# Optimization experiments

Hardware: AMD Instinct MI355X
Metric: run time of the kernel (lower is better)

## Reference

```python
import jax, jax.numpy as jnp
import numpy as np

NUM_CLASSES = 21
NEGPOS_RATIO = 3
B, P = 64, 24564


def setup_inputs() -> dict:
    key = jax.random.key(0)
    ks = jax.random.split(key, 10)
    return {
        "loc_data": jax.random.normal(ks[0], (B, P, 4), jnp.float32),
        "conf_data": jax.random.normal(ks[1], (B, P, NUM_CLASSES), jnp.float32),
        "has_lp_data": jax.random.normal(ks[2], (B, P, 2), jnp.float32),
        "size_lp_data": jax.random.normal(ks[3], (B, P, 2), jnp.float32),
        "offset_data": jax.random.normal(ks[4], (B, P, 2), jnp.float32),
        "loc_t": jax.random.normal(ks[5], (B, P, 4), jnp.float32),
        "conf_t": jax.random.randint(ks[6], (B, P), 0, NUM_CLASSES, jnp.int64),
        "has_lp_t": jax.random.randint(ks[7], (B, P), 0, 2, jnp.int64),
        "size_lp_t": jax.random.normal(ks[8], (B, P, 2), jnp.float32),
        "offset_t": jax.random.normal(ks[9], (B, P, 2), jnp.float32),
    }


def _smooth_l1_sum(p, t, mask):
    # sum-reduced smooth L1 (beta=1) over elements selected by mask
    d = jnp.abs(p - t)
    l = jnp.where(d < 1.0, 0.5 * d * d, d - 0.5)
    return jnp.sum(l * mask)


def _ce_per_row(logits, labels):
    # per-row cross entropy: logsumexp(logits) - logits[label]
    lse = jax.nn.logsumexp(logits, axis=-1)
    g = jnp.take_along_axis(logits, labels[..., None], axis=-1)[..., 0]
    return lse - g


def reference(loc_data, conf_data, has_lp_data, size_lp_data, offset_data,
              loc_t, conf_t, has_lp_t, size_lp_t, offset_t):
    dt = loc_data.dtype
    num_priors = conf_data.shape[1]
    pos = conf_t > 0                                  # [B,P]
    posf = pos.astype(dt)[..., None]                  # [B,P,1]

    # localization loss over positives
    loss_l = _smooth_l1_sum(loc_data, loc_t, posf)

    # size / offset losses over positives, gated by has_lp flag
    hlp = has_lp_t.astype(dt)[..., None]              # [B,P,1]
    loss_size_lp = _smooth_l1_sum(size_lp_data * hlp, size_lp_t * hlp, posf)
    loss_offset = _smooth_l1_sum(offset_data * hlp, offset_t * hlp, posf)

    # hard negative mining on per-prior conf CE
    ce = _ce_per_row(conf_data, conf_t)               # [B,P]
    ce_mine = jnp.where(pos, 0.0, ce)
    loss_idx = jnp.argsort(-ce_mine, axis=1)          # descending sort indices
    idx_rank = jnp.argsort(loss_idx, axis=1)          # rank of each prior
    num_pos = jnp.sum(pos, axis=1, keepdims=True)     # [B,1]
    num_neg = jnp.clip(NEGPOS_RATIO * num_pos, None, num_priors - 1)
    neg = idx_rank < num_neg                          # [B,P]
    sel = (pos | neg).astype(dt)

    loss_c = jnp.sum(ce * sel)
    loss_has_lp = jnp.sum(_ce_per_row(has_lp_data, has_lp_t) * sel)

    N = jnp.sum(pos).astype(dt)
    return (loss_l / N, loss_c / N, loss_size_lp / N,
            loss_offset / N, loss_has_lp / N)
```

## Files before the change

### kernel.cpp

```cpp
#include <hip/hip_runtime.h>
#include <stdint.h>

#define NC 21
#define BATCH 64
#define PRI 24564
#define NROWS (BATCH * PRI)
#define SLABS 32
#define SLABR 768
#define GBLK (BATCH * SLABS)
#define SENT 0xFFFFFFFFu

typedef float f4a4 __attribute__((ext_vector_type(4), aligned(4)));

__device__ __forceinline__ float sl1f(float p, float t) {
    float d = fabsf(p - t);
    return d < 1.0f ? 0.5f * d * d : d - 0.5f;
}

__device__ __forceinline__ unsigned int f2k(float v) {
    unsigned int u = __float_as_uint(v);
    return (u & 0x80000000u) ? ~u : (u | 0x80000000u);
}

__device__ __forceinline__ unsigned int chkey(float2 ch) {
    unsigned hb = __float_as_uint(ch.y);
    return (hb & 0x80000000u) ? 0x80000000u : f2k(ch.x);
}

__device__ __forceinline__ double blockReduce(double v, double* sred) {
    #pragma unroll
    for (int off = 32; off > 0; off >>= 1)
        v += __shfl_down(v, off, 64);
    const int wid = threadIdx.x >> 6, lane = threadIdx.x & 63;
    __syncthreads();
    if (lane == 0) sred[wid] = v;
    __syncthreads();
    double r = 0.0;
    if (threadIdx.x == 0) r = sred[0] + sred[1] + sred[2] + sred[3];
    return r;
}

__global__ __launch_bounds__(256, 4) void k_main(
    const float* __restrict__ loc_data, const float* __restrict__ conf_data,
    const float* __restrict__ has_lp_data, const float* __restrict__ size_lp_data,
    const float* __restrict__ offset_data, const float* __restrict__ loc_t,
    const int* __restrict__ conf_t, const int* __restrict__ has_lp_t,
    const float* __restrict__ size_lp_t, const float* __restrict__ offset_t,
    float2* __restrict__ ws_ch, int* __restrict__ numpos, double* __restrict__ part,
    int* __restrict__ ghist1)
{
    __shared__ int hist[4096];
    __shared__ double sred[4];
    const int tid = threadIdx.x;
    const int b = blockIdx.x >> 5, s = blockIdx.x & 31;
    for (int k = tid; k < 4096; k += 256) hist[k] = 0;
    __syncthreads();

    int pr[3]; bool vld[3];
    #pragma unroll
    for (int i = 0; i < 3; ++i) {
        int p = s * SLABR + i * 256 + tid;
        vld[i] = p < PRI;
        pr[i] = vld[i] ? p : PRI - 1;
    }
    const unsigned rb = (unsigned)b * PRI;

    int ct[3];
    #pragma unroll
    for (int i = 0; i < 3; ++i) ct[i] = conf_t[rb + pr[i]];
    f4a4 cw[3][5]; float c20[3], gg[3];
    #pragma unroll
    for (int i = 0; i < 3; ++i) {
        const float* crow = conf_data + (long)(rb + pr[i]) * NC;
        #pragma unroll
        for (int j = 0; j < 5; ++j) cw[i][j] = ((const f4a4*)crow)[j];
        c20[i] = crow[20];
        gg[i] = crow[ct[i]];
    }
    float ce[3];
    #pragma unroll
    for (int i = 0; i < 3; ++i) {
        float m = c20[i];
        #pragma unroll
        for (int j = 0; j < 5; ++j)
            m = fmaxf(m, fmaxf(fmaxf(cw[i][j].x, cw[i][j].y), fmaxf(cw[i][j].z, cw[i][j].w)));
        float sum = __expf(c20[i] - m);
        #pragma unroll
        for (int j = 0; j < 5; ++j)
            sum += __expf(cw[i][j].x - m) + __expf(cw[i][j].y - m)
                 + __expf(cw[i][j].z - m) + __expf(cw[i][j].w - m);
        ce[i] = m + __logf(sum) - gg[i];
    }
    #pragma unroll
    for (int i = 0; i < 3; ++i) {
        if (vld[i] && ct[i] <= 0) {
            unsigned key = f2k(ce[i]);
            if (key != 0x80000000u) atomicAdd(&hist[key >> 20], 1);
        }
    }

    int hl[3]; float4 lp[3], lt[3]; float2 sp2[3], st2[3], op2[3], ot2[3], hh[3];
    #pragma unroll
    for (int i = 0; i < 3; ++i) {
        const unsigned r = rb + pr[i];
        hl[i] = has_lp_t[r];
        lp[i] = ((const float4*)loc_data)[r];
        lt[i] = ((const float4*)loc_t)[r];
        sp2[i] = ((const float2*)size_lp_data)[r];
        st2[i] = ((const float2*)size_lp_t)[r];
        op2[i] = ((const float2*)offset_data)[r];
        ot2[i] = ((const float2*)offset_t)[r];
        hh[i] = ((const float2*)has_lp_data)[r];
    }
    double aL = 0.0, aS = 0.0, aO = 0.0;
    int myp = 0;
    #pragma unroll
    for (int i = 0; i < 3; ++i) {
        const bool pos = ct[i] > 0;
        float ll = sl1f(lp[i].x, lt[i].x) + sl1f(lp[i].y, lt[i].y)
                 + sl1f(lp[i].z, lt[i].z) + sl1f(lp[i].w, lt[i].w);
        float ls = sl1f(sp2[i].x, st2[i].x) + sl1f(sp2[i].y, st2[i].y);
        float lo = sl1f(op2[i].x, ot2[i].x) + sl1f(op2[i].y, ot2[i].y);
        const float pf = (vld[i] && pos) ? 1.f : 0.f;
        const float hf = (hl[i] != 0) ? 1.f : 0.f;
        aL += (double)(pf * ll);
        aS += (double)(pf * hf * ls);
        aO += (double)(pf * hf * lo);
        float hm = fmaxf(hh[i].x, hh[i].y);
        float hs = __expf(hh[i].x - hm) + __expf(hh[i].y - hm);
        float hlce = fmaxf(hm + __logf(hs) - (hl[i] != 0 ? hh[i].y : hh[i].x), 0.0f);
        unsigned hb = __float_as_uint(hlce) | (pos ? 0x80000000u : 0u);
        if (vld[i]) ws_ch[rb + pr[i]] = make_float2(ce[i], __uint_as_float(hb));
        myp += (vld[i] && pos) ? 1 : 0;
    }

    double v;
    v = blockReduce(aL, sred); if (tid == 0) part[0 * GBLK + blockIdx.x] = v;
    v = blockReduce(aS, sred); if (tid == 0) part[1 * GBLK + blockIdx.x] = v;
    v = blockReduce(aO, sred); if (tid == 0) part[2 * GBLK + blockIdx.x] = v;
    v = blockReduce((double)myp, sred);
    if (tid == 0 && v > 0.0) atomicAdd(&numpos[b], (int)(v + 0.5));

    __syncthreads();
    for (int k = tid; k < 4096; k += 256) {
        int h = hist[k];
        if (h) atomicAdd(&ghist1[(b << 12) + k], h);
    }
}

__global__ __launch_bounds__(256) void k_pick0(
    const int* __restrict__ ghist1, const int* __restrict__ numpos,
    unsigned* __restrict__ prefix_io, int* __restrict__ rem_io,
    unsigned* __restrict__ selT, int* __restrict__ needed)
{
    const int b = blockIdx.x, tid = threadIdx.x;
    __shared__ int sct[256];
    __shared__ unsigned s_dig;
    __shared__ int s_rem;

    int K = 3 * numpos[b]; if (K > PRI - 1) K = PRI - 1;

    int h[16];
    const int* g = ghist1 + (b << 12) + tid * 16;
    int ctn = 0;
    #pragma unroll
    for (int j = 0; j < 16; ++j) { h[j] = g[j]; ctn += h[j]; }
    sct[tid] = ctn;
    __syncthreads();
    #pragma unroll
    for (int off = 1; off < 256; off <<= 1) {
        int v = (tid + off < 256) ? sct[tid + off] : 0;
        __syncthreads();
        sct[tid] += v;
        __syncthreads();
    }
    const int M = sct[0];

    if (K <= 0) {
        if (tid == 0) { selT[b] = 0xFFFFFFFFu; needed[b] = 0; rem_io[b] = 0; prefix_io[b] = SENT; }
        return;
    }
    if (K > M) {
        if (tid == 0) { selT[b] = 0x80000000u; needed[b] = K - M; rem_io[b] = 0; prefix_io[b] = SENT; }
        return;
    }
    const int Safter = (tid < 255) ? sct[tid + 1] : 0;
    int cum = Safter;
    #pragma unroll
    for (int j = 15; j >= 0; --j) {
        int c2 = cum + h[j];
        if (c2 >= K && cum < K) { s_dig = (unsigned)(tid * 16 + j); s_rem = K - cum; }
        cum = c2;
    }
    __syncthreads();
    if (tid == 0) { prefix_io[b] = s_dig; rem_io[b] = s_rem; }
}

template<int MSHIFT, int BSHIFT>
__global__ __launch_bounds__(256) void k_hist(
    const float2* __restrict__ ws_ch, const unsigned* __restrict__ prefix_io,
    int* __restrict__ ghist)
{
    const int b = blockIdx.x >> 5, s = blockIdx.x & 31;
    const unsigned pref = prefix_io[b];
    if (pref == SENT) return;
    __shared__ int hist[1024];
    const int tid = threadIdx.x;
    for (int k = tid; k < 1024; k += 256) hist[k] = 0;
    __syncthreads();
    #pragma unroll
    for (int i = 0; i < 3; ++i) {
        const int p = s * SLABR + i * 256 + tid;
        if (p < PRI) {
            unsigned key = chkey(ws_ch[(unsigned)b * PRI + p]);
            if (key != 0x80000000u && (key >> MSHIFT) == pref)
                atomicAdd(&hist[(key >> BSHIFT) & 1023], 1);
        }
    }
    __syncthreads();
    for (int k = tid; k < 1024; k += 256) {
        int h = hist[k];
        if (h) atomicAdd(&ghist[(b << 10) + k], h);
    }
}

template<int ROUND>
__global__ __launch_bounds__(256) void k_pickR(
    const int* __restrict__ ghist, unsigned* __restrict__ prefix_io,
    int* __restrict__ rem_io, unsigned* __restrict__ selT, int* __restrict__ needed)
{
    const int b = blockIdx.x, tid = threadIdx.x;
    const int rem = rem_io[b];
    if (rem <= 0) return;
    __shared__ int sct[256];
    __shared__ unsigned s_dig;
    __shared__ int s_rem;
    int h[4];
    const int* g = ghist + (b << 10) + tid * 4;
    int ctn = 0;
    #pragma unroll
    for (int j = 0; j < 4; ++j) { h[j] = g[j]; ctn += h[j]; }
    sct[tid] = ctn;
    __syncthreads();
    #pragma unroll
    for (int off = 1; off < 256; off <<= 1) {
        int v = (tid + off < 256) ? sct[tid + off] : 0;
        __syncthreads();
        sct[tid] += v;
        __syncthreads();
    }
    const int Safter = (tid < 255) ? sct[tid + 1] : 0;
    int cum = Safter;
    #pragma unroll
    for (int j = 3; j >= 0; --j) {
        int c2 = cum + h[j];
        if (c2 >= rem && cum < rem) { s_dig = (unsigned)(tid * 4 + j); s_rem = rem - cum; }
        cum = c2;
    }
    __syncthreads();
    if (tid == 0) {
        if (ROUND == 1) { prefix_io[b] = (prefix_io[b] << 10) | s_dig; rem_io[b] = s_rem; }
        else            { selT[b] = (prefix_io[b] << 10) | s_dig;      needed[b] = s_rem; }
    }
}

__global__ __launch_bounds__(256) void k_sel2(
    const float2* __restrict__ ws_ch, const unsigned* __restrict__ selT,
    int* __restrict__ cntT, double* __restrict__ sums)
{
    __shared__ double sred[4];
    const int tid = threadIdx.x;
    const int b = blockIdx.x >> 5, s = blockIdx.x & 31;
    const unsigned T = selT[b];
    double aC = 0.0, aH = 0.0, tC = 0.0, tH = 0.0, cc = 0.0;
    #pragma unroll
    for (int i = 0; i < 3; ++i) {
        const int p = s * SLABR + i * 256 + tid;
        if (p < PRI) {
            float2 ch = ws_ch[(unsigned)b * PRI + p];
            unsigned hb = __float_as_uint(ch.y);
            const bool pos = (hb >> 31) != 0;
            const unsigned key = pos ? 0x80000000u : f2k(ch.x);
            const float hlv = __uint_as_float(hb & 0x7fffffffu);
            if (pos || key > T) { aC += (double)ch.x; aH += (double)hlv; }
            if (key == T) {
                cc += 1.0;
                if (!pos) { tC += (double)ch.x; tH += (double)hlv; }
            }
        }
    }
    double v;
    v = blockReduce(aC, sred); if (tid == 0) sums[0 * GBLK + blockIdx.x] = v;
    v = blockReduce(aH, sred); if (tid == 0) sums[1 * GBLK + blockIdx.x] = v;
    v = blockReduce(tC, sred); if (tid == 0) sums[2 * GBLK + blockIdx.x] = v;
    v = blockReduce(tH, sred); if (tid == 0) sums[3 * GBLK + blockIdx.x] = v;
    v = blockReduce(cc, sred); if (tid == 0) cntT[blockIdx.x] = (int)(v + 0.5);
}

__global__ __launch_bounds__(256) void k_cut(
    const float2* __restrict__ ws_ch, const unsigned* __restrict__ selT,
    const int* __restrict__ needed, const int* __restrict__ cntT,
    const double* __restrict__ sums, double* __restrict__ lossCH)
{
    const int b = blockIdx.x, tid = threadIdx.x;
    __shared__ double sred[4];
    __shared__ int scnt_s[32];
    __shared__ int s_sl, s_loc, s_found;
    __shared__ int wtot[4];
    const int need = needed[b];
    const unsigned T = selT[b];

    if (tid < 32) scnt_s[tid] = cntT[b * 32 + tid];
    __syncthreads();
    if (tid == 0) {
        int sl = 32, loc = 0, cum = 0;
        if (need > 0) {
            for (int s2 = 0; s2 < 32; ++s2) {
                int c2 = scnt_s[s2];
                if (cum + c2 >= need) { sl = s2; loc = need - cum; break; }
                cum += c2;
            }
        }
        s_sl = sl; s_loc = loc; s_found = -1;
    }
    __syncthreads();
    const int sl = s_sl, loc = s_loc;

    double aC = 0.0, aH = 0.0;
    if (tid < 32) {
        aC = sums[0 * GBLK + b * 32 + tid] + (tid < sl ? sums[2 * GBLK + b * 32 + tid] : 0.0);
        aH = sums[1 * GBLK + b * 32 + tid] + (tid < sl ? sums[3 * GBLK + b * 32 + tid] : 0.0);
    }
    double totC = blockReduce(aC, sred);
    double totH = blockReduce(aH, sred);

    if (sl < 32) {
        int run = 0;
        for (int i = 0; i < 3; ++i) {
            const int p = sl * SLABR + i * 256 + tid;
            bool eq = false;
            if (p < PRI) eq = (chkey(ws_ch[(unsigned)b * PRI + p]) == T);
            const unsigned long long m = __ballot(eq);
            const int lane = tid & 63, wid = tid >> 6;
            if (lane == 0) wtot[wid] = __popcll(m);
            const int mex = __popcll(m & ((1ull << lane) - 1ull));
            __syncthreads();
            int woff = 0;
            for (int w = 0; w < wid; ++w) woff += wtot[w];
            if (eq && (run + woff + mex + 1 == loc)) s_found = p;
            __syncthreads();
            run += wtot[0] + wtot[1] + wtot[2] + wtot[3];
            __syncthreads();
        }
        const int cutoff = s_found;
        double pC = 0.0, pH = 0.0;
        for (int i = 0; i < 3; ++i) {
            const int p = sl * SLABR + i * 256 + tid;
            if (p < PRI && p <= cutoff) {
                float2 ch = ws_ch[(unsigned)b * PRI + p];
                unsigned hb = __float_as_uint(ch.y);
                const bool pos = (hb >> 31) != 0;
                const unsigned key = pos ? 0x80000000u : f2k(ch.x);
                if (!pos && key == T) {
                    pC += (double)ch.x;
                    pH += (double)__uint_as_float(hb & 0x7fffffffu);
                }
            }
        }
        double v1 = blockReduce(pC, sred);
        double v2 = blockReduce(pH, sred);
        if (tid == 0) { totC += v1; totH += v2; }
    }
    if (tid == 0) { lossCH[b] = totC; lossCH[64 + b] = totH; }
}

__global__ __launch_bounds__(256) void k_final(
    const double* __restrict__ part, const int* __restrict__ numpos,
    const double* __restrict__ lossCH, float* __restrict__ out)
{
    __shared__ double sred[4];
    const int tid = threadIdx.x;
    double s[3];
    #pragma unroll
    for (int k = 0; k < 3; ++k) {
        double a = 0.0;
        for (int t = tid; t < GBLK; t += 256) a += part[k * GBLK + t];
        s[k] = blockReduce(a, sred);
    }
    double lc = (tid < BATCH) ? lossCH[tid] : 0.0;
    lc = blockReduce(lc, sred);
    double lh = (tid < BATCH) ? lossCH[64 + tid] : 0.0;
    lh = blockReduce(lh, sred);
    double n = (tid < BATCH) ? (double)numpos[tid] : 0.0;
    n = blockReduce(n, sred);
    if (tid == 0) {
        out[0] = (float)(s[0] / n);
        out[1] = (float)(lc / n);
        out[2] = (float)(s[1] / n);
        out[3] = (float)(s[2] / n);
        out[4] = (float)(lh / n);
    }
}

extern "C" void kernel_launch(void* const* d_in, const int* in_sizes, int n_in,
                              void* d_out, int out_size, void* d_ws, size_t ws_size,
                              hipStream_t stream)
{
    const float* loc_data     = (const float*)d_in[0];
    const float* conf_data    = (const float*)d_in[1];
    const float* has_lp_data  = (const float*)d_in[2];
    const float* size_lp_data = (const float*)d_in[3];
    const float* offset_data  = (const float*)d_in[4];
    const float* loc_t        = (const float*)d_in[5];
    const int*   conf_t       = (const int*)d_in[6];
    const int*   has_lp_t     = (const int*)d_in[7];
    const float* size_lp_t    = (const float*)d_in[8];
    const float* offset_t     = (const float*)d_in[9];
    float* out = (float*)d_out;

    char* ws = (char*)d_ws;
    int* numpos      = (int*)(ws + 0);
    unsigned* selT   = (unsigned*)(ws + 256);
    int* needed      = (int*)(ws + 512);
    unsigned* prefix = (unsigned*)(ws + 768);
    int* rem         = (int*)(ws + 1024);
    int* cntT        = (int*)(ws + 1536);
    double* part     = (double*)(ws + 16384);
    double* sums     = (double*)(ws + 65536);
    double* lossCH   = (double*)(ws + 131072);
    int* ghist1      = (int*)(ws + 132096);
    int* ghist2      = (int*)(ws + 1180672);
    int* ghist3      = (int*)(ws + 1442816);
    float2* ws_ch    = (float2*)(ws + 1704960);

    hipMemsetAsync(ws, 0, 256, stream);
    hipMemsetAsync(ws + 132096, 0, 1572864, stream);

    k_main<<<GBLK, 256, 0, stream>>>(loc_data, conf_data, has_lp_data, size_lp_data,
                                     offset_data, loc_t, conf_t, has_lp_t,
                                     size_lp_t, offset_t, ws_ch, numpos, part, ghist1);
    k_pick0<<<BATCH, 256, 0, stream>>>(ghist1, numpos, prefix, rem, selT, needed);
    k_hist<20, 10><<<GBLK, 256, 0, stream>>>(ws_ch, prefix, ghist2);
    k_pickR<1><<<BATCH, 256, 0, stream>>>(ghist2, prefix, rem, selT, needed);
    k_hist<10, 0><<<GBLK, 256, 0, stream>>>(ws_ch, prefix, ghist3);
    k_pickR<2><<<BATCH, 256, 0, stream>>>(ghist3, prefix, rem, selT, needed);
    k_sel2<<<GBLK, 256, 0, stream>>>(ws_ch, selT, cntT, sums);
    k_cut<<<BATCH, 256, 0, stream>>>(ws_ch, selT, needed, cntT, sums, lossCH);
    k_final<<<1, 256, 0, stream>>>(part, numpos, lossCH, out);
}
```

Measured before the change: 337.5 us.

## Fuse radix-select rounds and cutoff reduction into one per-batch kernel

Replaces the chain of pick/hist/select/cut kernels with a single kernel that launches one 256-thread block per batch row. The block runs both refinement histogram passes in shared memory, sums the selected CE and has_lp values, and finds the tie cutoff with a chunked prefix scan. This removes six kernel launches, the global histograms for rounds two and three, and their memset. In exchange, only 64 blocks do all the post-main work, each rereading its 24564-entry row up to about five times, so parallelism on the GPU drops sharply.

```diff
diff --git a/kernel.cpp b/kernel.cpp
--- a/kernel.cpp
+++ b/kernel.cpp
@@ -8,7 +8,7 @@
 #define SLABS 32
 #define SLABR 768
 #define GBLK (BATCH * SLABS)
-#define SENT 0xFFFFFFFFu
+#define CHUNK 96
 
 typedef float f4a4 __attribute__((ext_vector_type(4), aligned(4)));
 
@@ -148,24 +148,29 @@
     }
 }
 
-__global__ __launch_bounds__(256) void k_pick0(
-    const int* __restrict__ ghist1, const int* __restrict__ numpos,
-    unsigned* __restrict__ prefix_io, int* __restrict__ rem_io,
-    unsigned* __restrict__ selT, int* __restrict__ needed)
+__global__ __launch_bounds__(256) void k_batch(
+    const float2* __restrict__ ws_ch, const int* __restrict__ ghist1,
+    const int* __restrict__ numpos, double* __restrict__ lossCH)
 {
     const int b = blockIdx.x, tid = threadIdx.x;
     __shared__ int sct[256];
+    __shared__ int shist[1024];
+    __shared__ double sred[4];
     __shared__ unsigned s_dig;
     __shared__ int s_rem;
+    __shared__ int s_cut;
+
+    const float2* row = ws_ch + (unsigned)b * PRI;
 
     int K = 3 * numpos[b]; if (K > PRI - 1) K = PRI - 1;
-
     int h[16];
-    const int* g = ghist1 + (b << 12) + tid * 16;
-    int ctn = 0;
-    #pragma unroll
-    for (int j = 0; j < 16; ++j) { h[j] = g[j]; ctn += h[j]; }
-    sct[tid] = ctn;
+    {
+        const int* g = ghist1 + (b << 12) + tid * 16;
+        int ctn = 0;
+        #pragma unroll
+        for (int j = 0; j < 16; ++j) { h[j] = g[j]; ctn += h[j]; }
+        sct[tid] = ctn;
+    }
     __syncthreads();
     #pragma unroll
     for (int off = 1; off < 256; off <<= 1) {
@@ -176,201 +181,149 @@
     }
     const int M = sct[0];
 
+    unsigned T; int need;
     if (K <= 0) {
-        if (tid == 0) { selT[b] = 0xFFFFFFFFu; needed[b] = 0; rem_io[b] = 0; prefix_io[b] = SENT; }
-        return;
-    }
-    if (K > M) {
-        if (tid == 0) { selT[b] = 0x80000000u; needed[b] = K - M; rem_io[b] = 0; prefix_io[b] = SENT; }
-        return;
-    }
-    const int Safter = (tid < 255) ? sct[tid + 1] : 0;
-    int cum = Safter;
-    #pragma unroll
-    for (int j = 15; j >= 0; --j) {
-        int c2 = cum + h[j];
-        if (c2 >= K && cum < K) { s_dig = (unsigned)(tid * 16 + j); s_rem = K - cum; }
-        cum = c2;
-    }
-    __syncthreads();
-    if (tid == 0) { prefix_io[b] = s_dig; rem_io[b] = s_rem; }
-}
-
-template<int MSHIFT, int BSHIFT>
-__global__ __launch_bounds__(256) void k_hist(
-    const float2* __restrict__ ws_ch, const unsigned* __restrict__ prefix_io,
-    int* __restrict__ ghist)
-{
-    const int b = blockIdx.x >> 5, s = blockIdx.x & 31;
-    const unsigned pref = prefix_io[b];
-    if (pref == SENT) return;
-    __shared__ int hist[1024];
-    const int tid = threadIdx.x;
-    for (int k = tid; k < 1024; k += 256) hist[k] = 0;
-    __syncthreads();
-    #pragma unroll
-    for (int i = 0; i < 3; ++i) {
-        const int p = s * SLABR + i * 256 + tid;
-        if (p < PRI) {
-            unsigned key = chkey(ws_ch[(unsigned)b * PRI + p]);
-            if (key != 0x80000000u && (key >> MSHIFT) == pref)
-                atomicAdd(&hist[(key >> BSHIFT) & 1023], 1);
-        }
-    }
-    __syncthreads();
-    for (int k = tid; k < 1024; k += 256) {
-        int h = hist[k];
-        if (h) atomicAdd(&ghist[(b << 10) + k], h);
-    }
-}
-
-template<int ROUND>
-__global__ __launch_bounds__(256) void k_pickR(
-    const int* __restrict__ ghist, unsigned* __restrict__ prefix_io,
-    int* __restrict__ rem_io, unsigned* __restrict__ selT, int* __restrict__ needed)
-{
-    const int b = blockIdx.x, tid = threadIdx.x;
-    const int rem = rem_io[b];
-    if (rem <= 0) return;
-    __shared__ int sct[256];
-    __shared__ unsigned s_dig;
-    __shared__ int s_rem;
-    int h[4];
-    const int* g = ghist + (b << 10) + tid * 4;
-    int ctn = 0;
-    #pragma unroll
-    for (int j = 0; j < 4; ++j) { h[j] = g[j]; ctn += h[j]; }
-    sct[tid] = ctn;
+        T = 0xFFFFFFFFu; need = 0;
+    } else if (K > M) {
+        T = 0x80000000u; need = K - M;
+    } else {
+        const int Safter = (tid < 255) ? sct[tid + 1] : 0;
+        int cum = Safter;
+        #pragma unroll
+        for (int j = 15; j >= 0; --j) {
+            int c2 = cum + h[j];
+            if (c2 >= K && cum < K) { s_dig = (unsigned)(tid * 16 + j); s_rem = K - cum; }
+            cum = c2;
+        }
+        __syncthreads();
+        unsigned pref = s_dig; int rem = s_rem;
+
+        for (int k = tid; k < 1024; k += 256) shist[k] = 0;
+        __syncthreads();
+        for (int p = tid; p < PRI; p += 256) {
+            unsigned key = chkey(row[p]);
+            if (key != 0x80000000u && (key >> 20) == pref)
+                atomicAdd(&shist[(key >> 10) & 1023], 1);
+        }
+        __syncthreads();
+        {
+            int h4[4]; int c4 = 0;
+            #pragma unroll
+            for (int j = 0; j < 4; ++j) { h4[j] = shist[tid * 4 + j]; c4 += h4[j]; }
+            __syncthreads();
+            sct[tid] = c4;
+            __syncthreads();
+            #pragma unroll
+            for (int off = 1; off < 256; off <<= 1) {
+                int v = (tid + off < 256) ? sct[tid + off] : 0;
+                __syncthreads();
+                sct[tid] += v;
+                __syncthreads();
+            }
+            const int Sa = (tid < 255) ? sct[tid + 1] : 0;
+            int cum2 = Sa;
+            #pragma unroll
+            for (int j = 3; j >= 0; --j) {
+                int c2 = cum2 + h4[j];
+                if (c2 >= rem && cum2 < rem) { s_dig = (unsigned)(tid * 4 + j); s_rem = rem - cum2; }
+                cum2 = c2;
+            }
+            __syncthreads();
+        }
+        pref = (pref << 10) | s_dig; rem = s_rem;
+        __syncthreads();
+
+        for (int k = tid; k < 1024; k += 256) shist[k] = 0;
+        __syncthreads();
+        for (int p = tid; p < PRI; p += 256) {
+            unsigned key = chkey(row[p]);
+            if (key != 0x80000000u && (key >> 10) == pref)
+                atomicAdd(&shist[key & 1023], 1);
+        }
+        __syncthreads();
+        {
+            int h4[4]; int c4 = 0;
+            #pragma unroll
+            for (int j = 0; j < 4; ++j) { h4[j] = shist[tid * 4 + j]; c4 += h4[j]; }
+            __syncthreads();
+            sct[tid] = c4;
+            __syncthreads();
+            #pragma unroll
+            for (int off = 1; off < 256; off <<= 1) {
+                int v = (tid + off < 256) ? sct[tid + off] : 0;
+                __syncthreads();
+                sct[tid] += v;
+                __syncthreads();
+            }
+            const int Sa = (tid < 255) ? sct[tid + 1] : 0;
+            int cum2 = Sa;
+            #pragma unroll
+            for (int j = 3; j >= 0; --j) {
+                int c2 = cum2 + h4[j];
+                if (c2 >= rem && cum2 < rem) { s_dig = (unsigned)(tid * 4 + j); s_rem = rem - cum2; }
+                cum2 = c2;
+            }
+            __syncthreads();
+        }
+        T = (pref << 10) | s_dig; need = s_rem;
+        __syncthreads();
+    }
+
+    double aC = 0.0, aH = 0.0;
+    for (int p = tid; p < PRI; p += 256) {
+        float2 ch = row[p];
+        unsigned hb = __float_as_uint(ch.y);
+        const bool pos = (hb >> 31) != 0;
+        const unsigned key = pos ? 0x80000000u : f2k(ch.x);
+        const float hlv = __uint_as_float(hb & 0x7fffffffu);
+        if (pos || key > T) { aC += (double)ch.x; aH += (double)hlv; }
+    }
+
+    if (tid == 0) s_cut = -1;
+    __syncthreads();
+    const int c0 = tid * CHUNK;
+    const int c1 = (c0 + CHUNK < PRI) ? c0 + CHUNK : PRI;
+    int tcnt = 0;
+    if (need > 0) {
+        for (int p = c0; p < c1; ++p) tcnt += (chkey(row[p]) == T) ? 1 : 0;
+    }
+    sct[tid] = tcnt;
     __syncthreads();
     #pragma unroll
     for (int off = 1; off < 256; off <<= 1) {
-        int v = (tid + off < 256) ? sct[tid + off] : 0;
+        int v = (tid >= off) ? sct[tid - off] : 0;
         __syncthreads();
         sct[tid] += v;
         __syncthreads();
     }
-    const int Safter = (tid < 255) ? sct[tid + 1] : 0;
-    int cum = Safter;
-    #pragma unroll
-    for (int j = 3; j >= 0; --j) {
-        int c2 = cum + h[j];
-        if (c2 >= rem && cum < rem) { s_dig = (unsigned)(tid * 4 + j); s_rem = rem - cum; }
-        cum = c2;
-    }
-    __syncthreads();
-    if (tid == 0) {
-        if (ROUND == 1) { prefix_io[b] = (prefix_io[b] << 10) | s_dig; rem_io[b] = s_rem; }
-        else            { selT[b] = (prefix_io[b] << 10) | s_dig;      needed[b] = s_rem; }
-    }
-}
-
-__global__ __launch_bounds__(256) void k_sel2(
-    const float2* __restrict__ ws_ch, const unsigned* __restrict__ selT,
-    int* __restrict__ cntT, double* __restrict__ sums)
-{
-    __shared__ double sred[4];
-    const int tid = threadIdx.x;
-    const int b = blockIdx.x >> 5, s = blockIdx.x & 31;
-    const unsigned T = selT[b];
-    double aC = 0.0, aH = 0.0, tC = 0.0, tH = 0.0, cc = 0.0;
-    #pragma unroll
-    for (int i = 0; i < 3; ++i) {
-        const int p = s * SLABR + i * 256 + tid;
-        if (p < PRI) {
-            float2 ch = ws_ch[(unsigned)b * PRI + p];
-            unsigned hb = __float_as_uint(ch.y);
-            const bool pos = (hb >> 31) != 0;
-            const unsigned key = pos ? 0x80000000u : f2k(ch.x);
-            const float hlv = __uint_as_float(hb & 0x7fffffffu);
-            if (pos || key > T) { aC += (double)ch.x; aH += (double)hlv; }
+    if (need > 0) {
+        const int incl = sct[tid], excl = incl - tcnt;
+        if (excl < need && need <= incl) {
+            int want = need - excl, c = 0;
+            for (int p = c0; p < c1; ++p) {
+                if (chkey(row[p]) == T) { ++c; if (c == want) { s_cut = p; break; } }
+            }
+        }
+    }
+    __syncthreads();
+    const int cutoff = s_cut;
+
+    double tCn = 0.0, tHn = 0.0;
+    for (int p = tid; p <= cutoff; p += 256) {
+        float2 ch = row[p];
+        unsigned hb = __float_as_uint(ch.y);
+        const bool pos = (hb >> 31) != 0;
+        if (!pos) {
+            const unsigned key = f2k(ch.x);
             if (key == T) {
-                cc += 1.0;
-                if (!pos) { tC += (double)ch.x; tH += (double)hlv; }
-            }
-        }
-    }
-    double v;
-    v = blockReduce(aC, sred); if (tid == 0) sums[0 * GBLK + blockIdx.x] = v;
-    v = blockReduce(aH, sred); if (tid == 0) sums[1 * GBLK + blockIdx.x] = v;
-    v = blockReduce(tC, sred); if (tid == 0) sums[2 * GBLK + blockIdx.x] = v;
-    v = blockReduce(tH, sred); if (tid == 0) sums[3 * GBLK + blockIdx.x] = v;
-    v = blockReduce(cc, sred); if (tid == 0) cntT[blockIdx.x] = (int)(v + 0.5);
-}
-
-__global__ __launch_bounds__(256) void k_cut(
-    const float2* __restrict__ ws_ch, const unsigned* __restrict__ selT,
-    const int* __restrict__ needed, const int* __restrict__ cntT,
-    const double* __restrict__ sums, double* __restrict__ lossCH)
-{
-    const int b = blockIdx.x, tid = threadIdx.x;
-    __shared__ double sred[4];
-    __shared__ int scnt_s[32];
-    __shared__ int s_sl, s_loc, s_found;
-    __shared__ int wtot[4];
-    const int need = needed[b];
-    const unsigned T = selT[b];
-
-    if (tid < 32) scnt_s[tid] = cntT[b * 32 + tid];
-    __syncthreads();
-    if (tid == 0) {
-        int sl = 32, loc = 0, cum = 0;
-        if (need > 0) {
-            for (int s2 = 0; s2 < 32; ++s2) {
-                int c2 = scnt_s[s2];
-                if (cum + c2 >= need) { sl = s2; loc = need - cum; break; }
-                cum += c2;
-            }
-        }
-        s_sl = sl; s_loc = loc; s_found = -1;
-    }
-    __syncthreads();
-    const int sl = s_sl, loc = s_loc;
-
-    double aC = 0.0, aH = 0.0;
-    if (tid < 32) {
-        aC = sums[0 * GBLK + b * 32 + tid] + (tid < sl ? sums[2 * GBLK + b * 32 + tid] : 0.0);
-        aH = sums[1 * GBLK + b * 32 + tid] + (tid < sl ? sums[3 * GBLK + b * 32 + tid] : 0.0);
-    }
-    double totC = blockReduce(aC, sred);
-    double totH = blockReduce(aH, sred);
-
-    if (sl < 32) {
-        int run = 0;
-        for (int i = 0; i < 3; ++i) {
-            const int p = sl * SLABR + i * 256 + tid;
-            bool eq = false;
-            if (p < PRI) eq = (chkey(ws_ch[(unsigned)b * PRI + p]) == T);
-            const unsigned long long m = __ballot(eq);
-            const int lane = tid & 63, wid = tid >> 6;
-            if (lane == 0) wtot[wid] = __popcll(m);
-            const int mex = __popcll(m & ((1ull << lane) - 1ull));
-            __syncthreads();
-            int woff = 0;
-            for (int w = 0; w < wid; ++w) woff += wtot[w];
-            if (eq && (run + woff + mex + 1 == loc)) s_found = p;
-            __syncthreads();
-            run += wtot[0] + wtot[1] + wtot[2] + wtot[3];
-            __syncthreads();
-        }
-        const int cutoff = s_found;
-        double pC = 0.0, pH = 0.0;
-        for (int i = 0; i < 3; ++i) {
-            const int p = sl * SLABR + i * 256 + tid;
-            if (p < PRI && p <= cutoff) {
-                float2 ch = ws_ch[(unsigned)b * PRI + p];
-                unsigned hb = __float_as_uint(ch.y);
-                const bool pos = (hb >> 31) != 0;
-                const unsigned key = pos ? 0x80000000u : f2k(ch.x);
-                if (!pos && key == T) {
-                    pC += (double)ch.x;
-                    pH += (double)__uint_as_float(hb & 0x7fffffffu);
-                }
-            }
-        }
-        double v1 = blockReduce(pC, sred);
-        double v2 = blockReduce(pH, sred);
-        if (tid == 0) { totC += v1; totH += v2; }
-    }
+                tCn += (double)ch.x;
+                tHn += (double)__uint_as_float(hb & 0x7fffffffu);
+            }
+        }
+    }
+
+    double totC = blockReduce(aC + tCn, sred);
+    double totH = blockReduce(aH + tHn, sred);
     if (tid == 0) { lossCH[b] = totC; lossCH[64 + b] = totH; }
 }
 
@@ -420,31 +373,17 @@
 
     char* ws = (char*)d_ws;
     int* numpos      = (int*)(ws + 0);
-    unsigned* selT   = (unsigned*)(ws + 256);
-    int* needed      = (int*)(ws + 512);
-    unsigned* prefix = (unsigned*)(ws + 768);
-    int* rem         = (int*)(ws + 1024);
-    int* cntT        = (int*)(ws + 1536);
     double* part     = (double*)(ws + 16384);
-    double* sums     = (double*)(ws + 65536);
     double* lossCH   = (double*)(ws + 131072);
     int* ghist1      = (int*)(ws + 132096);
-    int* ghist2      = (int*)(ws + 1180672);
-    int* ghist3      = (int*)(ws + 1442816);
     float2* ws_ch    = (float2*)(ws + 1704960);
 
     hipMemsetAsync(ws, 0, 256, stream);
-    hipMemsetAsync(ws + 132096, 0, 1572864, stream);
+    hipMemsetAsync(ws + 132096, 0, 1048576, stream);
 
     k_main<<<GBLK, 256, 0, stream>>>(loc_data, conf_data, has_lp_data, size_lp_data,
                                      offset_data, loc_t, conf_t, has_lp_t,
                                      size_lp_t, offset_t, ws_ch, numpos, part, ghist1);
-    k_pick0<<<BATCH, 256, 0, stream>>>(ghist1, numpos, prefix, rem, selT, needed);
-    k_hist<20, 10><<<GBLK, 256, 0, stream>>>(ws_ch, prefix, ghist2);
-    k_pickR<1><<<BATCH, 256, 0, stream>>>(ghist2, prefix, rem, selT, needed);
-    k_hist<10, 0><<<GBLK, 256, 0, stream>>>(ws_ch, prefix, ghist3);
-    k_pickR<2><<<BATCH, 256, 0, stream>>>(ghist3, prefix, rem, selT, needed);
-    k_sel2<<<GBLK, 256, 0, stream>>>(ws_ch, selT, cntT, sums);
-    k_cut<<<BATCH, 256, 0, stream>>>(ws_ch, selT, needed, cntT, sums, lossCH);
+    k_batch<<<BATCH, 256, 0, stream>>>(ws_ch, ghist1, numpos, lossCH);
     k_final<<<1, 256, 0, stream>>>(part, numpos, lossCH, out);
 }
```

Result: slower. 385.8 us (+14.3%).

## Split main kernel and fuse radix-select passes into one per-batch kernel

Applied to the files above, without the earlier changes.

Splits the fused main kernel into a cross-entropy kernel and a smooth-L1 kernel, which write interleaved halves of the workspace. Global histogram atomics, the memsets and the separate pick/hist launches are replaced by a single per-batch k_thr kernel. That kernel does all three radix-select rounds in shared memory, rereading its batch row three times. Positive and candidate counts come from per-block partial sums instead of atomics. This cuts launches, memsets and global atomics, but runs the selection on only 64 blocks, each streaming about 200KB three times, so per-batch serial work grows.

```diff
diff --git a/kernel.cpp b/kernel.cpp
--- a/kernel.cpp
+++ b/kernel.cpp
@@ -4,7 +4,6 @@
 #define NC 21
 #define BATCH 64
 #define PRI 24564
-#define NROWS (BATCH * PRI)
 #define SLABS 32
 #define SLABR 768
 #define GBLK (BATCH * SLABS)
@@ -40,21 +39,13 @@
     return r;
 }
 
-__global__ __launch_bounds__(256, 4) void k_main(
-    const float* __restrict__ loc_data, const float* __restrict__ conf_data,
-    const float* __restrict__ has_lp_data, const float* __restrict__ size_lp_data,
-    const float* __restrict__ offset_data, const float* __restrict__ loc_t,
-    const int* __restrict__ conf_t, const int* __restrict__ has_lp_t,
-    const float* __restrict__ size_lp_t, const float* __restrict__ offset_t,
-    float2* __restrict__ ws_ch, int* __restrict__ numpos, double* __restrict__ part,
-    int* __restrict__ ghist1)
-{
-    __shared__ int hist[4096];
+__global__ __launch_bounds__(256, 4) void k_ce(
+    const float* __restrict__ conf_data, const int* __restrict__ conf_t,
+    float* __restrict__ wsf , double* __restrict__ partPN)
+{
     __shared__ double sred[4];
     const int tid = threadIdx.x;
     const int b = blockIdx.x >> 5, s = blockIdx.x & 31;
-    for (int k = tid; k < 4096; k += 256) hist[k] = 0;
-    __syncthreads();
 
     int pr[3]; bool vld[3];
     #pragma unroll
@@ -77,7 +68,7 @@
         c20[i] = crow[20];
         gg[i] = crow[ct[i]];
     }
-    float ce[3];
+    int myp = 0, myn = 0;
     #pragma unroll
     for (int i = 0; i < 3; ++i) {
         float m = c20[i];
@@ -89,20 +80,45 @@
         for (int j = 0; j < 5; ++j)
             sum += __expf(cw[i][j].x - m) + __expf(cw[i][j].y - m)
                  + __expf(cw[i][j].z - m) + __expf(cw[i][j].w - m);
-        ce[i] = m + __logf(sum) - gg[i];
-    }
-    #pragma unroll
-    for (int i = 0; i < 3; ++i) {
-        if (vld[i] && ct[i] <= 0) {
-            unsigned key = f2k(ce[i]);
-            if (key != 0x80000000u) atomicAdd(&hist[key >> 20], 1);
-        }
-    }
-
-    int hl[3]; float4 lp[3], lt[3]; float2 sp2[3], st2[3], op2[3], ot2[3], hh[3];
+        const float ce = m + __logf(sum) - gg[i];
+        if (vld[i]) wsf[2u * (rb + pr[i])] = ce;
+        const bool pos = ct[i] > 0;
+        myp += (vld[i] && pos) ? 1 : 0;
+        myn += (vld[i] && !pos && f2k(ce) != 0x80000000u) ? 1 : 0;
+    }
+    double v;
+    v = blockReduce((double)myp, sred);
+    if (tid == 0) partPN[0 * GBLK + blockIdx.x] = v;
+    v = blockReduce((double)myn, sred);
+    if (tid == 0) partPN[1 * GBLK + blockIdx.x] = v;
+}
+
+__global__ __launch_bounds__(256, 4) void k_sl1(
+    const float* __restrict__ loc_data, const float* __restrict__ has_lp_data,
+    const float* __restrict__ size_lp_data, const float* __restrict__ offset_data,
+    const float* __restrict__ loc_t, const int* __restrict__ conf_t,
+    const int* __restrict__ has_lp_t, const float* __restrict__ size_lp_t,
+    const float* __restrict__ offset_t,
+    float* __restrict__ wsf , double* __restrict__ partL)
+{
+    __shared__ double sred[4];
+    const int tid = threadIdx.x;
+    const int b = blockIdx.x >> 5, s = blockIdx.x & 31;
+
+    int pr[3]; bool vld[3];
+    #pragma unroll
+    for (int i = 0; i < 3; ++i) {
+        int p = s * SLABR + i * 256 + tid;
+        vld[i] = p < PRI;
+        pr[i] = vld[i] ? p : PRI - 1;
+    }
+    const unsigned rb = (unsigned)b * PRI;
+
+    int ct[3], hl[3]; float4 lp[3], lt[3]; float2 sp2[3], st2[3], op2[3], ot2[3], hh[3];
     #pragma unroll
     for (int i = 0; i < 3; ++i) {
         const unsigned r = rb + pr[i];
+        ct[i] = conf_t[r];
         hl[i] = has_lp_t[r];
         lp[i] = ((const float4*)loc_data)[r];
         lt[i] = ((const float4*)loc_t)[r];
@@ -113,7 +129,6 @@
         hh[i] = ((const float2*)has_lp_data)[r];
     }
     double aL = 0.0, aS = 0.0, aO = 0.0;
-    int myp = 0;
     #pragma unroll
     for (int i = 0; i < 3; ++i) {
         const bool pos = ct[i] > 0;
@@ -130,138 +145,138 @@
         float hs = __expf(hh[i].x - hm) + __expf(hh[i].y - hm);
         float hlce = fmaxf(hm + __logf(hs) - (hl[i] != 0 ? hh[i].y : hh[i].x), 0.0f);
         unsigned hb = __float_as_uint(hlce) | (pos ? 0x80000000u : 0u);
-        if (vld[i]) ws_ch[rb + pr[i]] = make_float2(ce[i], __uint_as_float(hb));
-        myp += (vld[i] && pos) ? 1 : 0;
-    }
-
+        if (vld[i]) wsf[2u * (rb + pr[i]) + 1u] = __uint_as_float(hb);
+    }
     double v;
-    v = blockReduce(aL, sred); if (tid == 0) part[0 * GBLK + blockIdx.x] = v;
-    v = blockReduce(aS, sred); if (tid == 0) part[1 * GBLK + blockIdx.x] = v;
-    v = blockReduce(aO, sred); if (tid == 0) part[2 * GBLK + blockIdx.x] = v;
-    v = blockReduce((double)myp, sred);
-    if (tid == 0 && v > 0.0) atomicAdd(&numpos[b], (int)(v + 0.5));
-
-    __syncthreads();
-    for (int k = tid; k < 4096; k += 256) {
-        int h = hist[k];
-        if (h) atomicAdd(&ghist1[(b << 12) + k], h);
-    }
-}
-
-__global__ __launch_bounds__(256) void k_pick0(
-    const int* __restrict__ ghist1, const int* __restrict__ numpos,
-    unsigned* __restrict__ prefix_io, int* __restrict__ rem_io,
+    v = blockReduce(aL, sred); if (tid == 0) partL[0 * GBLK + blockIdx.x] = v;
+    v = blockReduce(aS, sred); if (tid == 0) partL[1 * GBLK + blockIdx.x] = v;
+    v = blockReduce(aO, sred); if (tid == 0) partL[2 * GBLK + blockIdx.x] = v;
+}
+
+__global__ __launch_bounds__(256) void k_thr(
+    const float2* __restrict__ ws_ch, const double* __restrict__ partPN,
     unsigned* __restrict__ selT, int* __restrict__ needed)
 {
     const int b = blockIdx.x, tid = threadIdx.x;
+    __shared__ double sred[4];
+    __shared__ int shist[4096];
     __shared__ int sct[256];
     __shared__ unsigned s_dig;
     __shared__ int s_rem;
-
-    int K = 3 * numpos[b]; if (K > PRI - 1) K = PRI - 1;
-
-    int h[16];
-    const int* g = ghist1 + (b << 12) + tid * 16;
-    int ctn = 0;
-    #pragma unroll
-    for (int j = 0; j < 16; ++j) { h[j] = g[j]; ctn += h[j]; }
-    sct[tid] = ctn;
-    __syncthreads();
-    #pragma unroll
-    for (int off = 1; off < 256; off <<= 1) {
-        int v = (tid + off < 256) ? sct[tid + off] : 0;
-        __syncthreads();
-        sct[tid] += v;
-        __syncthreads();
-    }
-    const int M = sct[0];
-
-    if (K <= 0) {
-        if (tid == 0) { selT[b] = 0xFFFFFFFFu; needed[b] = 0; rem_io[b] = 0; prefix_io[b] = SENT; }
-        return;
-    }
-    if (K > M) {
-        if (tid == 0) { selT[b] = 0x80000000u; needed[b] = K - M; rem_io[b] = 0; prefix_io[b] = SENT; }
-        return;
-    }
-    const int Safter = (tid < 255) ? sct[tid + 1] : 0;
-    int cum = Safter;
-    #pragma unroll
-    for (int j = 15; j >= 0; --j) {
-        int c2 = cum + h[j];
-        if (c2 >= K && cum < K) { s_dig = (unsigned)(tid * 16 + j); s_rem = K - cum; }
-        cum = c2;
-    }
-    __syncthreads();
-    if (tid == 0) { prefix_io[b] = s_dig; rem_io[b] = s_rem; }
-}
-
-template<int MSHIFT, int BSHIFT>
-__global__ __launch_bounds__(256) void k_hist(
-    const float2* __restrict__ ws_ch, const unsigned* __restrict__ prefix_io,
-    int* __restrict__ ghist)
-{
-    const int b = blockIdx.x >> 5, s = blockIdx.x & 31;
-    const unsigned pref = prefix_io[b];
-    if (pref == SENT) return;
-    __shared__ int hist[1024];
-    const int tid = threadIdx.x;
-    for (int k = tid; k < 1024; k += 256) hist[k] = 0;
-    __syncthreads();
-    #pragma unroll
-    for (int i = 0; i < 3; ++i) {
-        const int p = s * SLABR + i * 256 + tid;
-        if (p < PRI) {
-            unsigned key = chkey(ws_ch[(unsigned)b * PRI + p]);
-            if (key != 0x80000000u && (key >> MSHIFT) == pref)
-                atomicAdd(&hist[(key >> BSHIFT) & 1023], 1);
-        }
-    }
-    __syncthreads();
-    for (int k = tid; k < 1024; k += 256) {
-        int h = hist[k];
-        if (h) atomicAdd(&ghist[(b << 10) + k], h);
-    }
-}
-
-template<int ROUND>
-__global__ __launch_bounds__(256) void k_pickR(
-    const int* __restrict__ ghist, unsigned* __restrict__ prefix_io,
-    int* __restrict__ rem_io, unsigned* __restrict__ selT, int* __restrict__ needed)
-{
-    const int b = blockIdx.x, tid = threadIdx.x;
-    const int rem = rem_io[b];
-    if (rem <= 0) return;
-    __shared__ int sct[256];
-    __shared__ unsigned s_dig;
-    __shared__ int s_rem;
-    int h[4];
-    const int* g = ghist + (b << 10) + tid * 4;
-    int ctn = 0;
-    #pragma unroll
-    for (int j = 0; j < 4; ++j) { h[j] = g[j]; ctn += h[j]; }
-    sct[tid] = ctn;
-    __syncthreads();
-    #pragma unroll
-    for (int off = 1; off < 256; off <<= 1) {
-        int v = (tid + off < 256) ? sct[tid + off] : 0;
-        __syncthreads();
-        sct[tid] += v;
-        __syncthreads();
-    }
-    const int Safter = (tid < 255) ? sct[tid + 1] : 0;
-    int cum = Safter;
-    #pragma unroll
-    for (int j = 3; j >= 0; --j) {
-        int c2 = cum + h[j];
-        if (c2 >= rem && cum < rem) { s_dig = (unsigned)(tid * 4 + j); s_rem = rem - cum; }
-        cum = c2;
-    }
-    __syncthreads();
+    __shared__ int s_K, s_M;
+
+    double np = blockReduce((tid < SLABS) ? partPN[0 * GBLK + b * SLABS + tid] : 0.0, sred);
+    double mm = blockReduce((tid < SLABS) ? partPN[1 * GBLK + b * SLABS + tid] : 0.0, sred);
     if (tid == 0) {
-        if (ROUND == 1) { prefix_io[b] = (prefix_io[b] << 10) | s_dig; rem_io[b] = s_rem; }
-        else            { selT[b] = (prefix_io[b] << 10) | s_dig;      needed[b] = s_rem; }
-    }
+        int K = 3 * (int)(np + 0.5); if (K > PRI - 1) K = PRI - 1;
+        s_K = K; s_M = (int)(mm + 0.5);
+    }
+    __syncthreads();
+    const int K = s_K, M = s_M;
+
+    if (K <= 0) { if (tid == 0) { selT[b] = SENT; needed[b] = 0; } return; }
+    if (K > M)  { if (tid == 0) { selT[b] = 0x80000000u; needed[b] = K - M; } return; }
+
+    const float2* row = ws_ch + (unsigned)b * PRI;
+    for (int k = tid; k < 4096; k += 256) shist[k] = 0;
+    __syncthreads();
+    for (int p = tid; p < PRI; p += 256) {
+        unsigned key = chkey(row[p]);
+        if (key != 0x80000000u) atomicAdd(&shist[key >> 20], 1);
+    }
+    __syncthreads();
+    {
+        int h[16]; int ctn = 0;
+        #pragma unroll
+        for (int j = 0; j < 16; ++j) { h[j] = shist[tid * 16 + j]; ctn += h[j]; }
+        sct[tid] = ctn;
+        __syncthreads();
+        #pragma unroll
+        for (int off = 1; off < 256; off <<= 1) {
+            int v = (tid + off < 256) ? sct[tid + off] : 0;
+            __syncthreads();
+            sct[tid] += v;
+            __syncthreads();
+        }
+        const int Sa = (tid < 255) ? sct[tid + 1] : 0;
+        int cum = Sa;
+        #pragma unroll
+        for (int j = 15; j >= 0; --j) {
+            int c2 = cum + h[j];
+            if (c2 >= K && cum < K) { s_dig = (unsigned)(tid * 16 + j); s_rem = K - cum; }
+            cum = c2;
+        }
+        __syncthreads();
+    }
+    unsigned pref = s_dig; int rem = s_rem;
+    __syncthreads();
+
+    for (int k = tid; k < 1024; k += 256) shist[k] = 0;
+    __syncthreads();
+    for (int p = tid; p < PRI; p += 256) {
+        unsigned key = chkey(row[p]);
+        if (key != 0x80000000u && (key >> 20) == pref)
+            atomicAdd(&shist[(key >> 10) & 1023], 1);
+    }
+    __syncthreads();
+    {
+        int h4[4]; int c4 = 0;
+        #pragma unroll
+        for (int j = 0; j < 4; ++j) { h4[j] = shist[tid * 4 + j]; c4 += h4[j]; }
+        sct[tid] = c4;
+        __syncthreads();
+        #pragma unroll
+        for (int off = 1; off < 256; off <<= 1) {
+            int v = (tid + off < 256) ? sct[tid + off] : 0;
+            __syncthreads();
+            sct[tid] += v;
+            __syncthreads();
+        }
+        const int Sa = (tid < 255) ? sct[tid + 1] : 0;
+        int cum = Sa;
+        #pragma unroll
+        for (int j = 3; j >= 0; --j) {
+            int c2 = cum + h4[j];
+            if (c2 >= rem && cum < rem) { s_dig = (unsigned)(tid * 4 + j); s_rem = rem - cum; }
+            cum = c2;
+        }
+        __syncthreads();
+    }
+    pref = (pref << 10) | s_dig; rem = s_rem;
+    __syncthreads();
+
+    for (int k = tid; k < 1024; k += 256) shist[k] = 0;
+    __syncthreads();
+    for (int p = tid; p < PRI; p += 256) {
+        unsigned key = chkey(row[p]);
+        if (key != 0x80000000u && (key >> 10) == pref)
+            atomicAdd(&shist[key & 1023], 1);
+    }
+    __syncthreads();
+    {
+        int h4[4]; int c4 = 0;
+        #pragma unroll
+        for (int j = 0; j < 4; ++j) { h4[j] = shist[tid * 4 + j]; c4 += h4[j]; }
+        sct[tid] = c4;
+        __syncthreads();
+        #pragma unroll
+        for (int off = 1; off < 256; off <<= 1) {
+            int v = (tid + off < 256) ? sct[tid + off] : 0;
+            __syncthreads();
+            sct[tid] += v;
+            __syncthreads();
+        }
+        const int Sa = (tid < 255) ? sct[tid + 1] : 0;
+        int cum = Sa;
+        #pragma unroll
+        for (int j = 3; j >= 0; --j) {
+            int c2 = cum + h4[j];
+            if (c2 >= rem && cum < rem) { s_dig = (unsigned)(tid * 4 + j); s_rem = rem - cum; }
+            cum = c2;
+        }
+        __syncthreads();
+    }
+    if (tid == 0) { selT[b] = (pref << 10) | s_dig; needed[b] = s_rem; }
 }
 
 __global__ __launch_bounds__(256) void k_sel2(
@@ -375,7 +390,7 @@
 }
 
 __global__ __launch_bounds__(256) void k_final(
-    const double* __restrict__ part, const int* __restrict__ numpos,
+    const double* __restrict__ partL, const double* __restrict__ partPN,
     const double* __restrict__ lossCH, float* __restrict__ out)
 {
     __shared__ double sred[4];
@@ -384,15 +399,16 @@
     #pragma unroll
     for (int k = 0; k < 3; ++k) {
         double a = 0.0;
-        for (int t = tid; t < GBLK; t += 256) a += part[k * GBLK + t];
+        for (int t = tid; t < GBLK; t += 256) a += partL[k * GBLK + t];
         s[k] = blockReduce(a, sred);
     }
+    double a = 0.0;
+    for (int t = tid; t < GBLK; t += 256) a += partPN[t];
+    double n = blockReduce(a, sred);
     double lc = (tid < BATCH) ? lossCH[tid] : 0.0;
     lc = blockReduce(lc, sred);
     double lh = (tid < BATCH) ? lossCH[64 + tid] : 0.0;
     lh = blockReduce(lh, sred);
-    double n = (tid < BATCH) ? (double)numpos[tid] : 0.0;
-    n = blockReduce(n, sred);
     if (tid == 0) {
         out[0] = (float)(s[0] / n);
         out[1] = (float)(lc / n);
@@ -419,32 +435,22 @@
     float* out = (float*)d_out;
 
     char* ws = (char*)d_ws;
-    int* numpos      = (int*)(ws + 0);
-    unsigned* selT   = (unsigned*)(ws + 256);
+    unsigned* selT   = (unsigned*)(ws + 0);
     int* needed      = (int*)(ws + 512);
-    unsigned* prefix = (unsigned*)(ws + 768);
-    int* rem         = (int*)(ws + 1024);
     int* cntT        = (int*)(ws + 1536);
-    double* part     = (double*)(ws + 16384);
-    double* sums     = (double*)(ws + 65536);
-    double* lossCH   = (double*)(ws + 131072);
-    int* ghist1      = (int*)(ws + 132096);
-    int* ghist2      = (int*)(ws + 1180672);
-    int* ghist3      = (int*)(ws + 1442816);
+    double* partL    = (double*)(ws + 16384);
+    double* partPN   = (double*)(ws + 65536);
+    double* sums     = (double*)(ws + 131072);
+    double* lossCH   = (double*)(ws + 262144);
     float2* ws_ch    = (float2*)(ws + 1704960);
-
-    hipMemsetAsync(ws, 0, 256, stream);
-    hipMemsetAsync(ws + 132096, 0, 1572864, stream);
-
-    k_main<<<GBLK, 256, 0, stream>>>(loc_data, conf_data, has_lp_data, size_lp_data,
-                                     offset_data, loc_t, conf_t, has_lp_t,
-                                     size_lp_t, offset_t, ws_ch, numpos, part, ghist1);
-    k_pick0<<<BATCH, 256, 0, stream>>>(ghist1, numpos, prefix, rem, selT, needed);
-    k_hist<20, 10><<<GBLK, 256, 0, stream>>>(ws_ch, prefix, ghist2);
-    k_pickR<1><<<BATCH, 256, 0, stream>>>(ghist2, prefix, rem, selT, needed);
-    k_hist<10, 0><<<GBLK, 256, 0, stream>>>(ws_ch, prefix, ghist3);
-    k_pickR<2><<<BATCH, 256, 0, stream>>>(ghist3, prefix, rem, selT, needed);
+    float*  wsf      = (float*)ws_ch;
+
+    k_ce<<<GBLK, 256, 0, stream>>>(conf_data, conf_t, wsf, partPN);
+    k_sl1<<<GBLK, 256, 0, stream>>>(loc_data, has_lp_data, size_lp_data, offset_data,
+                                    loc_t, conf_t, has_lp_t, size_lp_t, offset_t,
+                                    wsf, partL);
+    k_thr<<<BATCH, 256, 0, stream>>>(ws_ch, partPN, selT, needed);
     k_sel2<<<GBLK, 256, 0, stream>>>(ws_ch, selT, cntT, sums);
     k_cut<<<BATCH, 256, 0, stream>>>(ws_ch, selT, needed, cntT, sums, lossCH);
-    k_final<<<1, 256, 0, stream>>>(part, numpos, lossCH, out);
-}
+    k_final<<<1, 256, 0, stream>>>(partL, partPN, lossCH, out);
+}
```

Measured after the change: 327.8 us. -2.9%, faster.
